# Optimization experiments

Hardware: AMD Instinct MI355X
Metric: run time of the kernel (lower is better)

Reference implementation:

```python
import jax, jax.numpy as jnp
import numpy as np

L, K, D, V, S, B = 2, 4, 1024, 32000, 1024, 2

# Constant neighbor influence from the 2x2 grid (success_rate==0.5 for fresh blocks)
_pos = np.array([[0, 0], [0, 1], [1, 0], [1, 1]], dtype=np.float64)
_dist = np.sqrt(((_pos[:, None, :] - _pos[None, :, :]) ** 2).sum(-1))
_infl = np.where(np.eye(K, dtype=bool), 0.0, 0.5 / (1.0 + _dist)).sum(-1)
NEIGHBOR_SIG = jnp.asarray(1.0 / (1.0 + np.exp(-_infl)), dtype=jnp.float32)  # [K]


def _ln(x, g, b, eps=1e-5):
    mu = x.mean(-1, keepdims=True)
    var = ((x - mu) ** 2).mean(-1, keepdims=True)
    return (x - mu) / jnp.sqrt(var + eps) * g + b


def setup_inputs() -> dict:
    key = jax.random.key(0)
    ks = jax.random.split(key, 10)
    def n(k, shape, s):
        return jax.random.normal(k, shape, jnp.float32) * s
    return {
        "input_ids": jax.random.randint(ks[0], (B, S), 0, V),
        "embedding": n(ks[1], (V, D), 0.02),
        "pos_enc": n(ks[2], (S, D), 0.02),
        "torsion_field": jnp.zeros((D,), jnp.float32),
        "ln1_g": jnp.ones((L, D), jnp.float32),
        "ln1_b": jnp.zeros((L, D), jnp.float32),
        "base_W": n(ks[3], (L, D, D), 0.02),
        "blk_W1": n(ks[4], (L, K, D // 2, D), 0.02),
        "blk_W2": n(ks[5], (L, K, D, D // 2), 0.02),
        "blk_gate": n(ks[6], (L, K, D), 0.01),
        "prop_W": n(ks[7], (L, K, K), 0.5),
        "prop_b": jnp.zeros((L, K), jnp.float32),
        "ln2_g": jnp.ones((L, D), jnp.float32),
        "ln2_b": jnp.zeros((L, D), jnp.float32),
        "out_ln_g": jnp.ones((D,), jnp.float32),
        "out_ln_b": jnp.zeros((D,), jnp.float32),
        "lm_head_W": n(ks[8], (V, D), 0.02),
    }


def reference(input_ids, embedding, pos_enc, torsion_field, ln1_g, ln1_b,
              base_W, blk_W1, blk_W2, blk_gate, prop_W, prop_b,
              ln2_g, ln2_b, out_ln_g, out_ln_b, lm_head_W):
    h = embedding[input_ids] + pos_enc[None]  # [B,S,D]
    s = jnp.full((K,), 0.5, h.dtype)  # fresh blocks: success_rate = 0.5
    for l in range(L):
        # excitement (detached in torch via .item())
        exc0 = jax.nn.sigmoid(prop_W[l] @ s + prop_b[l])
        exc = jax.lax.stop_gradient(0.6 * exc0 + 0.4 * NEIGHBOR_SIG)  # [K]
        hn = _ln(h, ln1_g[l], ln1_b[l])
        base = hn @ base_W[l].T  # [B,S,D]
        # all K blocks are always loaded (min_blocks == max_blocks == 4)
        t = jnp.einsum('bsd,khd->bksh', hn, blk_W1[l])
        t = jax.nn.gelu(t, approximate=False)
        t = jnp.einsum('bksh,kdh->bksd', t, blk_W2[l])
        gate = jax.nn.sigmoid(blk_gate[l] + torsion_field)  # [K,D]
        t = t * gate[None, :, None, :]
        combined = jnp.einsum('bksd,k->bsd', t, exc) / exc.sum()
        h = h + (base + combined) * 0.3
        h = _ln(h, ln2_g[l], ln2_b[l])
    h = _ln(h, out_ln_g, out_ln_b)
    return h @ lm_head_W.T  # [B,S,V]
```

## Files before the change

kernel.cpp:

```cpp
#include <hip/hip_runtime.h>
#include <math.h>

typedef unsigned short u16;
typedef short s16x8 __attribute__((ext_vector_type(8)));
typedef float f32x4 __attribute__((ext_vector_type(4)));
typedef u16 u16x4 __attribute__((ext_vector_type(4)));

#define D 1024
#define MM 2048
#define HH 512
#define VV 32000

static __device__ __forceinline__ u16 f2bf(float f) {
    union { float f; unsigned int i; } c; c.f = f;
    unsigned int x = c.i;
    return (u16)((x + 0x7fffu + ((x >> 16) & 1u)) >> 16);
}
static __device__ __forceinline__ float sigm(float x) { return 1.0f / (1.0f + expf(-x)); }

static __device__ __forceinline__ void load_lds16(const u16* g, u16* l) {
    __builtin_amdgcn_global_load_lds(
        (const __attribute__((address_space(1))) unsigned int*)g,
        (__attribute__((address_space(3))) unsigned int*)l, 16, 0, 0);
}

__global__ __launch_bounds__(256) void cvt_kernel(const float* __restrict__ in,
                                                  u16* __restrict__ out, const int n4)
{
    for (int i = blockIdx.x * 256 + threadIdx.x; i < n4; i += gridDim.x * 256) {
        f32x4 v = __builtin_nontemporal_load((const f32x4*)in + i);
        u16x4 o;
#pragma unroll
        for (int j = 0; j < 4; j++) o[j] = f2bf(v[j]);
        ((u16x4*)out)[i] = o;
    }
}

__global__ __launch_bounds__(256) void cvtcat_kernel(const float* __restrict__ baseW,
    const float* __restrict__ W1, u16* __restrict__ out)
{
    const int N4 = 3072 * 1024 / 4, B4 = 1024 * 1024 / 4;
    for (int i = blockIdx.x * 256 + threadIdx.x; i < N4; i += gridDim.x * 256) {
        f32x4 v = (i < B4) ? __builtin_nontemporal_load((const f32x4*)baseW + i)
                           : __builtin_nontemporal_load((const f32x4*)W1 + (i - B4));
        u16x4 o;
#pragma unroll
        for (int j = 0; j < 4; j++) o[j] = f2bf(v[j]);
        ((u16x4*)out)[i] = o;
    }
}

__global__ __launch_bounds__(256) void embed_kernel(const int* __restrict__ ids,
    const float* __restrict__ emb, const float* __restrict__ pos, float* __restrict__ h)
{
    const int m = blockIdx.x;
    const int s = m & 1023;
    const long id = ids[m];
    const int d = threadIdx.x * 4;
    f32x4 ev = *(const f32x4*)&emb[id * D + d];
    f32x4 pv = *(const f32x4*)&pos[(long)s * D + d];
    f32x4 o;
#pragma unroll
    for (int i = 0; i < 4; i++) o[i] = ev[i] + pv[i];
    *(f32x4*)&h[(long)m * D + d] = o;
}

__global__ __launch_bounds__(256) void ln_bf16_kernel(const float* __restrict__ h,
    u16* __restrict__ out, const float* __restrict__ g, const float* __restrict__ b)
{
    const int row = blockIdx.x;
    const int d = threadIdx.x * 4;
    f32x4 x = *(const f32x4*)&h[(long)row * D + d];
    float s = x[0] + x[1] + x[2] + x[3];
    float ss = x[0]*x[0] + x[1]*x[1] + x[2]*x[2] + x[3]*x[3];
#pragma unroll
    for (int off = 32; off; off >>= 1) { s += __shfl_xor(s, off); ss += __shfl_xor(ss, off); }
    __shared__ float red[8];
    const int wid = threadIdx.x >> 6;
    if ((threadIdx.x & 63) == 0) { red[wid] = s; red[4 + wid] = ss; }
    __syncthreads();
    s = red[0] + red[1] + red[2] + red[3];
    ss = red[4] + red[5] + red[6] + red[7];
    const float mu = s * (1.0f / D);
    const float rstd = rsqrtf(ss * (1.0f / D) - mu * mu + 1e-5f);
    f32x4 gv = *(const f32x4*)&g[d];
    f32x4 bv = *(const f32x4*)&b[d];
    u16x4 o;
#pragma unroll
    for (int i = 0; i < 4; i++) o[i] = f2bf((x[i] - mu) * rstd * gv[i] + bv[i]);
    *(u16x4*)&out[(long)row * D + d] = o;
}

__global__ __launch_bounds__(256) void resln_kernel(float* __restrict__ h,
    const float* __restrict__ c, const float* __restrict__ g, const float* __restrict__ b)
{
    const int row = blockIdx.x;
    const int d = threadIdx.x * 4;
    f32x4 x = *(const f32x4*)&h[(long)row * D + d];
    f32x4 cv = *(const f32x4*)&c[(long)row * D + d];
#pragma unroll
    for (int i = 0; i < 4; i++) x[i] += 0.3f * cv[i];
    float s = x[0] + x[1] + x[2] + x[3];
    float ss = x[0]*x[0] + x[1]*x[1] + x[2]*x[2] + x[3]*x[3];
#pragma unroll
    for (int off = 32; off; off >>= 1) { s += __shfl_xor(s, off); ss += __shfl_xor(ss, off); }
    __shared__ float red[8];
    const int wid = threadIdx.x >> 6;
    if ((threadIdx.x & 63) == 0) { red[wid] = s; red[4 + wid] = ss; }
    __syncthreads();
    s = red[0] + red[1] + red[2] + red[3];
    ss = red[4] + red[5] + red[6] + red[7];
    const float mu = s * (1.0f / D);
    const float rstd = rsqrtf(ss * (1.0f / D) - mu * mu + 1e-5f);
    f32x4 gv = *(const f32x4*)&g[d];
    f32x4 bv = *(const f32x4*)&b[d];
    f32x4 o;
#pragma unroll
    for (int i = 0; i < 4; i++) o[i] = (x[i] - mu) * rstd * gv[i] + bv[i];
    *(f32x4*)&h[(long)row * D + d] = o;
}

__global__ void exc_kernel(const float* __restrict__ pW, const float* __restrict__ pb,
                           float* __restrict__ sc)
{
    if (threadIdx.x == 0 && blockIdx.x == 0) {
        const float NS = 1.0f / (1.0f + expf(-0.70710678118654752f));
        float e[4], sum = 0.0f;
        for (int k = 0; k < 4; k++) {
            float a = pb[k];
            for (int j = 0; j < 4; j++) a += 0.5f * pW[k * 4 + j];
            e[k] = 0.6f * sigm(a) + 0.4f * NS;
            sum += e[k];
        }
        for (int k = 0; k < 4; k++) sc[k] = e[k] / sum;
    }
}

__global__ __launch_bounds__(256) void scale_w2_kernel(
    const float* __restrict__ W2l, const float* __restrict__ gatel,
    const float* __restrict__ tors, const float* __restrict__ sc,
    u16* __restrict__ W2eff)
{
    const int n = blockIdx.x >> 1;
    const int half = blockIdx.x & 1;
    const int kh = half * 1024 + threadIdx.x * 4;
    const int k = kh >> 9;
    const int hh = kh & 511;
    const float f = sigm(gatel[k * D + n] + tors[n]) * sc[k];
    f32x4 w = __builtin_nontemporal_load((const f32x4*)&W2l[((long)k * D + n) * HH + hh]);
    u16x4 o;
#pragma unroll
    for (int i = 0; i < 4; i++) o[i] = f2bf(w[i] * f);
    *(u16x4*)&W2eff[(long)n * 2048 + kh] = o;
}

template<int EPI>
__global__ __launch_bounds__(256) void gemm_t(
    const u16* __restrict__ A, const u16* __restrict__ W,
    float* __restrict__ Cf, u16* __restrict__ Cb,
    const int Kloop, const int ldk, const long ldc)
{
    if (EPI == 4) { A += blockIdx.z * 512; W += blockIdx.z * 512; }

    const int gx = gridDim.x;
    const int nwg = gx * gridDim.y;
    int lin = blockIdx.y * gx + blockIdx.x;
    lin = (lin & 7) * (nwg >> 3) + (lin >> 3);
    const int bm = (lin % gx) * 128;
    const int bn = (lin / gx) * 128;

    __shared__ __align__(16) u16 AB[8192];

    const int tid = threadIdx.x, lane = tid & 63, w = tid >> 6;
    const int wm = w >> 1, wn = w & 1;
    const int l15 = lane & 15, lk8 = (lane >> 4) * 8;

    const u16* src[4];
    u16* dst[4];
#pragma unroll
    for (int ci = 0; ci < 4; ++ci) {
        const int c = w + ci * 4;
        src[ci] = (c < 8 ? A + (long)(bm + c * 16 + l15) * ldk
                         : W + (long)(bn + (c - 8) * 16 + l15) * ldk) + lk8;
        dst[ci] = AB + c * 512;
    }

    f32x4 acc[4][4];
#pragma unroll
    for (int i = 0; i < 4; ++i)
#pragma unroll
        for (int j = 0; j < 4; ++j) acc[i][j] = f32x4{0.f, 0.f, 0.f, 0.f};

    for (int k0 = 0; k0 < Kloop; k0 += 32) {
        __syncthreads();
#pragma unroll
        for (int ci = 0; ci < 4; ++ci) load_lds16(src[ci] + k0, dst[ci]);
        __syncthreads();
        s16x8 a[4], b[4];
#pragma unroll
        for (int i = 0; i < 4; ++i) a[i] = *(const s16x8*)(AB + (wm * 4 + i) * 512 + lane * 8);
#pragma unroll
        for (int j = 0; j < 4; ++j) b[j] = *(const s16x8*)(AB + (8 + wn * 4 + j) * 512 + lane * 8);
#pragma unroll
        for (int i = 0; i < 4; ++i)
#pragma unroll
            for (int j = 0; j < 4; ++j)
                acc[i][j] = __builtin_amdgcn_mfma_f32_16x16x32_bf16(a[i], b[j], acc[i][j], 0, 0, 0);
    }

    const int r0 = (lane >> 4) * 4;
#pragma unroll
    for (int i = 0; i < 4; ++i) {
#pragma unroll
        for (int j = 0; j < 4; ++j) {
            const int n = bn + wn * 64 + j * 16 + l15;
#pragma unroll
            for (int rr = 0; rr < 4; ++rr) {
                const int m = bm + wm * 64 + i * 16 + r0 + rr;
                const float v = acc[i][j][rr];
                if (EPI == 3) {
                    if (n < 1024) {
                        Cf[(long)m * 1024 + n] = v;
                    } else {
                        const float gel = 0.5f * v * (1.0f + erff(v * 0.70710678118654752f));
                        Cb[(long)m * 2048 + (n - 1024)] = f2bf(gel);
                    }
                } else {
                    atomicAdd(&Cf[(long)m * ldc + n], v);
                }
            }
        }
    }
}

#define AU16  16384
#define HALFU 8192
#define BB0   32768

__global__ __launch_bounds__(512, 2) void gemm256_kernel(
    const u16* __restrict__ Ag, const u16* __restrict__ Wg, float* __restrict__ C)
{
    __shared__ __align__(16) u16 lds[65536];

    const int nwg = gridDim.x * gridDim.y;
    int lin = blockIdx.y * gridDim.x + blockIdx.x;
    lin = (lin & 7) * (nwg >> 3) + (lin >> 3);
    const int bm = (lin & 7) * 256;
    const int bn = (lin >> 3) * 256;

    const int tid = threadIdx.x;
    const int lane = tid & 63;
    const int w = tid >> 6;
    const int wm = w >> 2;
    const int wn = w & 3;

    const u16* aSrc = Ag + (long)(bm + w * 16 + (lane & 15)) * 1024 + ((lane >> 4) * 8);
    const u16* bSrc = Wg + (long)(bn + w * 16 + (lane & 15)) * 1024 + ((lane >> 4) * 8);
    u16* aDst = lds + w * 1024;
    u16* bDst = lds + BB0 + w * 1024;

    auto stageA = [&](int kt, int b, int kk) {
        const long co = (long)kt * 64 + kk * 32;
        load_lds16(aSrc + co,               aDst + b * AU16 + kk * 512);
        load_lds16(aSrc + co + 128 * 1024L, aDst + b * AU16 + HALFU + kk * 512);
    };
    auto stageB = [&](int kt, int b, int kk) {
        const long co = (long)kt * 64 + kk * 32;
        load_lds16(bSrc + co,               bDst + b * AU16 + kk * 512);
        load_lds16(bSrc + co + 128 * 1024L, bDst + b * AU16 + HALFU + kk * 512);
    };

    const u16* aRd = lds + wm * HALFU + lane * 8;
    const u16* bRd = lds + BB0 + (wn >> 1) * HALFU + (wn & 1) * 4096 + lane * 8;

    f32x4 acc[8][4];
#pragma unroll
    for (int i = 0; i < 8; ++i)
#pragma unroll
        for (int j = 0; j < 4; ++j) acc[i][j] = f32x4{0.f, 0.f, 0.f, 0.f};

    s16x8 F0[12], F1[12];

    stageA(0, 0, 0); stageB(0, 0, 0);
    stageA(0, 0, 1); stageB(0, 0, 1);
    stageA(1, 1, 0); stageB(1, 1, 0);
    asm volatile("s_waitcnt vmcnt(4)" ::: "memory");
    __builtin_amdgcn_s_barrier();
    __builtin_amdgcn_sched_barrier(0);

#pragma unroll
    for (int i = 0; i < 8; ++i) F0[i] = *(const s16x8*)(aRd + i * 1024);
#pragma unroll
    for (int j = 0; j < 4; ++j) F0[8 + j] = *(const s16x8*)(bRd + j * 1024);

    auto phase = [&](int p, s16x8 (&fu)[12], s16x8 (&fl)[12]) {
        const int pr = p + 1;
        const int Tr = (pr >> 1) & 15, kkr = pr & 1, br = Tr & 1;
        const u16* aR = aRd + br * AU16 + kkr * 512;
        const u16* bR = bRd + br * AU16 + kkr * 512;
#pragma unroll
        for (int i = 0; i < 8; ++i) fl[i] = *(const s16x8*)(aR + i * 1024);
#pragma unroll
        for (int j = 0; j < 4; ++j) fl[8 + j] = *(const s16x8*)(bR + j * 1024);
        const int us = 6 + 2 * p;
        const int Ts = (us >> 2) & 15, kks = (us >> 1) & 1, bs = Ts & 1;
        stageA(Ts, bs, kks);
        stageB(Ts, bs, kks);
        __builtin_amdgcn_sched_barrier(0);
        __builtin_amdgcn_s_setprio(1);
#pragma unroll
        for (int j = 0; j < 4; ++j)
#pragma unroll
            for (int i = 0; i < 8; ++i)
                acc[i][j] = __builtin_amdgcn_mfma_f32_16x16x32_bf16(fu[i], fu[8 + j], acc[i][j], 0, 0, 0);
        __builtin_amdgcn_s_setprio(0);
        __builtin_amdgcn_sched_barrier(0);
        asm volatile("s_waitcnt vmcnt(4)" ::: "memory");
        __builtin_amdgcn_s_barrier();
        __builtin_amdgcn_sched_barrier(0);
    };

    for (int p = 0; p < 32; p += 2) {
        phase(p,     F0, F1);
        phase(p + 1, F1, F0);
    }

    asm volatile("s_waitcnt vmcnt(0)" ::: "memory");

    const int r0 = (lane >> 4) * 4;
    const int cl = lane & 15;
#pragma unroll
    for (int i = 0; i < 8; ++i)
#pragma unroll
        for (int j = 0; j < 4; ++j) {
            const long m = bm + wm * 128 + i * 16 + r0;
            const int n = bn + wn * 64 + j * 16 + cl;
#pragma unroll
            for (int rr = 0; rr < 4; ++rr)
                __builtin_nontemporal_store(acc[i][j][rr], &C[(m + rr) * (long)VV + n]);
        }
}

extern "C" void kernel_launch(void* const* d_in, const int* in_sizes, int n_in,
                              void* d_out, int out_size, void* d_ws, size_t ws_size,
                              hipStream_t stream)
{
    (void)in_sizes; (void)n_in; (void)out_size; (void)ws_size;
    const int*   ids   = (const int*)d_in[0];
    const float* emb   = (const float*)d_in[1];
    const float* pos   = (const float*)d_in[2];
    const float* tors  = (const float*)d_in[3];
    const float* ln1g  = (const float*)d_in[4];
    const float* ln1b  = (const float*)d_in[5];
    const float* baseW = (const float*)d_in[6];
    const float* W1    = (const float*)d_in[7];
    const float* W2    = (const float*)d_in[8];
    const float* gate  = (const float*)d_in[9];
    const float* propW = (const float*)d_in[10];
    const float* propb = (const float*)d_in[11];
    const float* ln2g  = (const float*)d_in[12];
    const float* ln2b  = (const float*)d_in[13];
    const float* outg  = (const float*)d_in[14];
    const float* outb  = (const float*)d_in[15];
    const float* lmW   = (const float*)d_in[16];

    char* ws = (char*)d_ws;
    float* h     = (float*)(ws);
    u16*   hn    = (u16*)  (ws + (8l  << 20));
    u16*   Wcat  = (u16*)  (ws + (12l << 20));
    float* C     = (float*)(ws + (18l << 20));
    u16*   t     = (u16*)  (ws + (26l << 20));
    u16*   W2eff = (u16*)  (ws + (34l << 20));
    float* sc    = (float*)(ws + (38l << 20));
    u16*   lmWbf = (u16*)  (ws + (12l << 20));

    embed_kernel<<<MM, 256, 0, stream>>>(ids, emb, pos, h);

    for (int l = 0; l < 2; l++) {
        exc_kernel<<<1, 64, 0, stream>>>(propW + l * 16, propb + l * 4, sc);
        ln_bf16_kernel<<<MM, 256, 0, stream>>>(h, hn, ln1g + (long)l * D, ln1b + (long)l * D);
        cvtcat_kernel<<<1024, 256, 0, stream>>>(
            baseW + (long)l * D * D, W1 + (long)l * 4 * HH * D, Wcat);
        scale_w2_kernel<<<2048, 256, 0, stream>>>(
            W2 + (long)l * 4 * D * HH, gate + (long)l * 4 * D, tors, sc, W2eff);
        gemm_t<3><<<dim3(16, 24), 256, 0, stream>>>(
            hn, Wcat, C, t, 1024, 1024, 0);
        gemm_t<4><<<dim3(16, 8, 4), 256, 0, stream>>>(
            t, W2eff, C, nullptr, 512, 2048, 1024);
        resln_kernel<<<MM, 256, 0, stream>>>(h, C, ln2g + (long)l * D, ln2b + (long)l * D);
    }

    ln_bf16_kernel<<<MM, 256, 0, stream>>>(h, hn, outg, outb);
    cvt_kernel<<<2048, 256, 0, stream>>>(lmW, lmWbf, VV * D / 4);
    gemm256_kernel<<<dim3(8, 125), 512, 0, stream>>>(hn, lmWbf, (float*)d_out);
}
```

Before: 442.3 us.

## Fuse layernorms into neighbors, inline excitement, split LM-head GEMM into two kernels

Embedding is fused with the first layernorm, and the residual layernorm is fused with the next layer's input layernorm (or the final output layernorm). The excitement scalar computation moves into the W2 scaling kernel, which removes several small kernel launches and extra passes over the hidden state. The LM-head GEMM is split into two launches: the existing kernel covers the first half of the vocabulary and a new gemmB variant, which keeps B fragments in registers, covers the rest. Output stores also change from nontemporal to regular stores. The split adds a second launch and a less-tested kernel, and the excitement math is now recomputed in every block.

```diff
diff --git a/kernel.cpp b/kernel.cpp
--- a/kernel.cpp
+++ b/kernel.cpp
@@ -50,8 +50,10 @@
     }
 }
 
-__global__ __launch_bounds__(256) void embed_kernel(const int* __restrict__ ids,
-    const float* __restrict__ emb, const float* __restrict__ pos, float* __restrict__ h)
+__global__ __launch_bounds__(256) void embed_ln_kernel(const int* __restrict__ ids,
+    const float* __restrict__ emb, const float* __restrict__ pos,
+    const float* __restrict__ g, const float* __restrict__ b,
+    float* __restrict__ h, u16* __restrict__ hn)
 {
     const int m = blockIdx.x;
     const int s = m & 1023;
@@ -59,40 +61,34 @@
     const int d = threadIdx.x * 4;
     f32x4 ev = *(const f32x4*)&emb[id * D + d];
     f32x4 pv = *(const f32x4*)&pos[(long)s * D + d];
-    f32x4 o;
-#pragma unroll
-    for (int i = 0; i < 4; i++) o[i] = ev[i] + pv[i];
-    *(f32x4*)&h[(long)m * D + d] = o;
-}
-
-__global__ __launch_bounds__(256) void ln_bf16_kernel(const float* __restrict__ h,
-    u16* __restrict__ out, const float* __restrict__ g, const float* __restrict__ b)
-{
-    const int row = blockIdx.x;
-    const int d = threadIdx.x * 4;
-    f32x4 x = *(const f32x4*)&h[(long)row * D + d];
-    float s = x[0] + x[1] + x[2] + x[3];
+    f32x4 x;
+#pragma unroll
+    for (int i = 0; i < 4; i++) x[i] = ev[i] + pv[i];
+    *(f32x4*)&h[(long)m * D + d] = x;
+
+    float sm = x[0] + x[1] + x[2] + x[3];
     float ss = x[0]*x[0] + x[1]*x[1] + x[2]*x[2] + x[3]*x[3];
 #pragma unroll
-    for (int off = 32; off; off >>= 1) { s += __shfl_xor(s, off); ss += __shfl_xor(ss, off); }
+    for (int off = 32; off; off >>= 1) { sm += __shfl_xor(sm, off); ss += __shfl_xor(ss, off); }
     __shared__ float red[8];
     const int wid = threadIdx.x >> 6;
-    if ((threadIdx.x & 63) == 0) { red[wid] = s; red[4 + wid] = ss; }
+    if ((threadIdx.x & 63) == 0) { red[wid] = sm; red[4 + wid] = ss; }
     __syncthreads();
-    s = red[0] + red[1] + red[2] + red[3];
+    sm = red[0] + red[1] + red[2] + red[3];
     ss = red[4] + red[5] + red[6] + red[7];
-    const float mu = s * (1.0f / D);
+    const float mu = sm * (1.0f / D);
     const float rstd = rsqrtf(ss * (1.0f / D) - mu * mu + 1e-5f);
     f32x4 gv = *(const f32x4*)&g[d];
     f32x4 bv = *(const f32x4*)&b[d];
     u16x4 o;
 #pragma unroll
     for (int i = 0; i < 4; i++) o[i] = f2bf((x[i] - mu) * rstd * gv[i] + bv[i]);
-    *(u16x4*)&out[(long)row * D + d] = o;
-}
-
-__global__ __launch_bounds__(256) void resln_kernel(float* __restrict__ h,
-    const float* __restrict__ c, const float* __restrict__ g, const float* __restrict__ b)
+    *(u16x4*)&hn[(long)m * D + d] = o;
+}
+
+__global__ __launch_bounds__(256) void resln2_kernel(float* __restrict__ h,
+    const float* __restrict__ c, const float* __restrict__ g2, const float* __restrict__ b2,
+    const float* __restrict__ gn, const float* __restrict__ bn_, u16* __restrict__ hn)
 {
     const int row = blockIdx.x;
     const int d = threadIdx.x * 4;
@@ -100,53 +96,63 @@
     f32x4 cv = *(const f32x4*)&c[(long)row * D + d];
 #pragma unroll
     for (int i = 0; i < 4; i++) x[i] += 0.3f * cv[i];
-    float s = x[0] + x[1] + x[2] + x[3];
+    float sm = x[0] + x[1] + x[2] + x[3];
     float ss = x[0]*x[0] + x[1]*x[1] + x[2]*x[2] + x[3]*x[3];
 #pragma unroll
-    for (int off = 32; off; off >>= 1) { s += __shfl_xor(s, off); ss += __shfl_xor(ss, off); }
+    for (int off = 32; off; off >>= 1) { sm += __shfl_xor(sm, off); ss += __shfl_xor(ss, off); }
     __shared__ float red[8];
     const int wid = threadIdx.x >> 6;
-    if ((threadIdx.x & 63) == 0) { red[wid] = s; red[4 + wid] = ss; }
+    if ((threadIdx.x & 63) == 0) { red[wid] = sm; red[4 + wid] = ss; }
     __syncthreads();
-    s = red[0] + red[1] + red[2] + red[3];
+    sm = red[0] + red[1] + red[2] + red[3];
     ss = red[4] + red[5] + red[6] + red[7];
-    const float mu = s * (1.0f / D);
-    const float rstd = rsqrtf(ss * (1.0f / D) - mu * mu + 1e-5f);
-    f32x4 gv = *(const f32x4*)&g[d];
-    f32x4 bv = *(const f32x4*)&b[d];
-    f32x4 o;
-#pragma unroll
-    for (int i = 0; i < 4; i++) o[i] = (x[i] - mu) * rstd * gv[i] + bv[i];
-    *(f32x4*)&h[(long)row * D + d] = o;
-}
-
-__global__ void exc_kernel(const float* __restrict__ pW, const float* __restrict__ pb,
-                           float* __restrict__ sc)
-{
-    if (threadIdx.x == 0 && blockIdx.x == 0) {
-        const float NS = 1.0f / (1.0f + expf(-0.70710678118654752f));
-        float e[4], sum = 0.0f;
-        for (int k = 0; k < 4; k++) {
-            float a = pb[k];
-            for (int j = 0; j < 4; j++) a += 0.5f * pW[k * 4 + j];
-            e[k] = 0.6f * sigm(a) + 0.4f * NS;
-            sum += e[k];
-        }
-        for (int k = 0; k < 4; k++) sc[k] = e[k] / sum;
-    }
-}
-
-__global__ __launch_bounds__(256) void scale_w2_kernel(
+    float mu = sm * (1.0f / D);
+    float rstd = rsqrtf(ss * (1.0f / D) - mu * mu + 1e-5f);
+    f32x4 g2v = *(const f32x4*)&g2[d];
+    f32x4 b2v = *(const f32x4*)&b2[d];
+    f32x4 y;
+#pragma unroll
+    for (int i = 0; i < 4; i++) y[i] = (x[i] - mu) * rstd * g2v[i] + b2v[i];
+    *(f32x4*)&h[(long)row * D + d] = y;
+
+    sm = y[0] + y[1] + y[2] + y[3];
+    ss = y[0]*y[0] + y[1]*y[1] + y[2]*y[2] + y[3]*y[3];
+#pragma unroll
+    for (int off = 32; off; off >>= 1) { sm += __shfl_xor(sm, off); ss += __shfl_xor(ss, off); }
+    __syncthreads();
+    if ((threadIdx.x & 63) == 0) { red[wid] = sm; red[4 + wid] = ss; }
+    __syncthreads();
+    sm = red[0] + red[1] + red[2] + red[3];
+    ss = red[4] + red[5] + red[6] + red[7];
+    mu = sm * (1.0f / D);
+    rstd = rsqrtf(ss * (1.0f / D) - mu * mu + 1e-5f);
+    f32x4 gnv = *(const f32x4*)&gn[d];
+    f32x4 bnv = *(const f32x4*)&bn_[d];
+    u16x4 o;
+#pragma unroll
+    for (int i = 0; i < 4; i++) o[i] = f2bf((y[i] - mu) * rstd * gnv[i] + bnv[i]);
+    *(u16x4*)&hn[(long)row * D + d] = o;
+}
+
+__global__ __launch_bounds__(256) void scale_w2x_kernel(
     const float* __restrict__ W2l, const float* __restrict__ gatel,
-    const float* __restrict__ tors, const float* __restrict__ sc,
-    u16* __restrict__ W2eff)
-{
+    const float* __restrict__ tors, const float* __restrict__ pW,
+    const float* __restrict__ pb, u16* __restrict__ W2eff)
+{
+    const float NS = 1.0f / (1.0f + expf(-0.70710678118654752f));
+    float e[4], sum = 0.0f;
+#pragma unroll
+    for (int k = 0; k < 4; k++) {
+        float a = pb[k] + 0.5f * (pW[k*4] + pW[k*4+1] + pW[k*4+2] + pW[k*4+3]);
+        e[k] = 0.6f * sigm(a) + 0.4f * NS;
+        sum += e[k];
+    }
     const int n = blockIdx.x >> 1;
     const int half = blockIdx.x & 1;
     const int kh = half * 1024 + threadIdx.x * 4;
     const int k = kh >> 9;
     const int hh = kh & 511;
-    const float f = sigm(gatel[k * D + n] + tors[n]) * sc[k];
+    const float f = sigm(gatel[k * D + n] + tors[n]) * (e[k] / sum);
     f32x4 w = __builtin_nontemporal_load((const f32x4*)&W2l[((long)k * D + n) * HH + hh]);
     u16x4 o;
 #pragma unroll
@@ -337,7 +343,102 @@
             const int n = bn + wn * 64 + j * 16 + cl;
 #pragma unroll
             for (int rr = 0; rr < 4; ++rr)
-                __builtin_nontemporal_store(acc[i][j][rr], &C[(m + rr) * (long)VV + n]);
+                C[(m + rr) * (long)VV + n] = acc[i][j][rr];
+        }
+}
+
+__global__ __launch_bounds__(512) void gemmB_kernel(
+    const u16* __restrict__ Ag, const u16* __restrict__ Wg, float* __restrict__ C,
+    const int bn0)
+{
+    __shared__ __align__(16) u16 ldsA[2][16384];
+
+    const int nwg = gridDim.x * gridDim.y;
+    int lin = blockIdx.y * gridDim.x + blockIdx.x;
+    lin = (lin & 7) * (nwg >> 3) + (lin >> 3);
+    const int bm = (lin & 7) * 256;
+    const int bn = bn0 + (lin >> 3) * 256;
+
+    const int lane = threadIdx.x & 63, w = threadIdx.x >> 6;
+    const int wm = w >> 2, wn = w & 3;
+    const int l15 = lane & 15, lk8 = (lane >> 4) * 8;
+
+    const u16* aS[4];
+#pragma unroll
+    for (int c = 0; c < 4; ++c) {
+        const int ch = 4 * w + c;
+        aS[c] = Ag + (long)(bm + (ch >> 1) * 16 + l15) * 1024 + (ch & 1) * 32 + lk8;
+    }
+    const u16* bP[4];
+#pragma unroll
+    for (int j = 0; j < 4; ++j)
+        bP[j] = Wg + (long)(bn + wn * 64 + j * 16 + l15) * 1024 + lk8;
+
+    f32x4 acc[8][4];
+#pragma unroll
+    for (int i = 0; i < 8; ++i)
+#pragma unroll
+        for (int j = 0; j < 4; ++j) acc[i][j] = f32x4{0.f, 0.f, 0.f, 0.f};
+
+    auto stageA = [&](int kt, int buf) {
+#pragma unroll
+        for (int c = 0; c < 4; ++c)
+            load_lds16(aS[c] + (long)kt * 64, &ldsA[buf][(4 * w + c) * 512]);
+    };
+    s16x8 B0[8], B1[8];
+    auto loadB = [&](int kt, s16x8 (&B)[8]) {
+#pragma unroll
+        for (int kk = 0; kk < 2; ++kk)
+#pragma unroll
+            for (int j = 0; j < 4; ++j)
+                B[kk * 4 + j] = *(const s16x8*)(bP[j] + (long)kt * 64 + kk * 32);
+    };
+    auto compute = [&](int buf, s16x8 (&B)[8]) {
+#pragma unroll
+        for (int kk = 0; kk < 2; ++kk) {
+            s16x8 af[8];
+#pragma unroll
+            for (int i = 0; i < 8; ++i)
+                af[i] = *(const s16x8*)(&ldsA[buf][((wm * 8 + i) * 2 + kk) * 512] + lane * 8);
+            __builtin_amdgcn_s_setprio(1);
+#pragma unroll
+            for (int j = 0; j < 4; ++j)
+#pragma unroll
+                for (int i = 0; i < 8; ++i)
+                    acc[i][j] = __builtin_amdgcn_mfma_f32_16x16x32_bf16(af[i], B[kk * 4 + j], acc[i][j], 0, 0, 0);
+            __builtin_amdgcn_s_setprio(0);
+        }
+    };
+
+    stageA(0, 0);
+    loadB(0, B0);
+    asm volatile("s_waitcnt vmcnt(8)" ::: "memory");
+    __syncthreads();
+
+    for (int kt = 0; kt < 16; kt += 2) {
+        if (kt + 1 < 16) { stageA(kt + 1, 1); loadB(kt + 1, B1); }
+        compute(0, B0);
+        asm volatile("s_waitcnt vmcnt(8)" ::: "memory");
+        __syncthreads();
+        if (kt + 2 < 16) { stageA(kt + 2, 0); loadB(kt + 2, B0); }
+        if (kt + 1 < 16) compute(1, B1);
+        asm volatile("s_waitcnt vmcnt(8)" ::: "memory");
+        __syncthreads();
+    }
+
+    asm volatile("s_waitcnt vmcnt(0)" ::: "memory");
+
+    const int r0 = (lane >> 4) * 4;
+    const int cl = lane & 15;
+#pragma unroll
+    for (int i = 0; i < 8; ++i)
+#pragma unroll
+        for (int j = 0; j < 4; ++j) {
+            const long m = bm + wm * 128 + i * 16 + r0;
+            const int n = bn + wn * 64 + j * 16 + cl;
+#pragma unroll
+            for (int rr = 0; rr < 4; ++rr)
+                C[(m + rr) * (long)VV + n] = acc[i][j][rr];
         }
 }
 
@@ -371,26 +472,24 @@
     float* C     = (float*)(ws + (18l << 20));
     u16*   t     = (u16*)  (ws + (26l << 20));
     u16*   W2eff = (u16*)  (ws + (34l << 20));
-    float* sc    = (float*)(ws + (38l << 20));
     u16*   lmWbf = (u16*)  (ws + (12l << 20));
 
-    embed_kernel<<<MM, 256, 0, stream>>>(ids, emb, pos, h);
+    embed_ln_kernel<<<MM, 256, 0, stream>>>(ids, emb, pos, ln1g, ln1b, h, hn);
 
     for (int l = 0; l < 2; l++) {
-        exc_kernel<<<1, 64, 0, stream>>>(propW + l * 16, propb + l * 4, sc);
-        ln_bf16_kernel<<<MM, 256, 0, stream>>>(h, hn, ln1g + (long)l * D, ln1b + (long)l * D);
         cvtcat_kernel<<<1024, 256, 0, stream>>>(
             baseW + (long)l * D * D, W1 + (long)l * 4 * HH * D, Wcat);
-        scale_w2_kernel<<<2048, 256, 0, stream>>>(
-            W2 + (long)l * 4 * D * HH, gate + (long)l * 4 * D, tors, sc, W2eff);
-        gemm_t<3><<<dim3(16, 24), 256, 0, stream>>>(
-            hn, Wcat, C, t, 1024, 1024, 0);
-        gemm_t<4><<<dim3(16, 8, 4), 256, 0, stream>>>(
-            t, W2eff, C, nullptr, 512, 2048, 1024);
-        resln_kernel<<<MM, 256, 0, stream>>>(h, C, ln2g + (long)l * D, ln2b + (long)l * D);
-    }
-
-    ln_bf16_kernel<<<MM, 256, 0, stream>>>(h, hn, outg, outb);
+        scale_w2x_kernel<<<2048, 256, 0, stream>>>(
+            W2 + (long)l * 4 * D * HH, gate + (long)l * 4 * D, tors,
+            propW + l * 16, propb + l * 4, W2eff);
+        gemm_t<3><<<dim3(16, 24), 256, 0, stream>>>(hn, Wcat, C, t, 1024, 1024, 0);
+        gemm_t<4><<<dim3(16, 8, 4), 256, 0, stream>>>(t, W2eff, C, nullptr, 512, 2048, 1024);
+        resln2_kernel<<<MM, 256, 0, stream>>>(
+            h, C, ln2g + (long)l * D, ln2b + (long)l * D,
+            l == 0 ? ln1g + D : outg, l == 0 ? ln1b + D : outb, hn);
+    }
+
     cvt_kernel<<<2048, 256, 0, stream>>>(lmW, lmWbf, VV * D / 4);
-    gemm256_kernel<<<dim3(8, 125), 512, 0, stream>>>(hn, lmWbf, (float*)d_out);
-}
+    gemm256_kernel<<<dim3(8, 62), 512, 0, stream>>>(hn, lmWbf, (float*)d_out);
+    gemmB_kernel<<<dim3(8, 63), 512, 0, stream>>>(hn, lmWbf, (float*)d_out, 15872);
+}
```

Result: slower. 512.9 us (+16.0%).
